# Optimization experiments

Hardware: AMD Instinct MI355X
Metric: run time of the kernel (lower is better)

Reference implementation:

```python
import jax, jax.numpy as jnp
import numpy as np

B, T, I, H = 256, 1024, 128, 256


def setup_inputs() -> dict:
    key = jax.random.key(0)
    ks = jax.random.split(key, 10)
    p = lambda k, shape: jax.random.normal(k, shape, dtype=jnp.float32) * 0.1
    return {
        "x": jax.random.normal(ks[0], (B, T, I), dtype=jnp.float32),
        # forget gate
        "f_wh": p(ks[1], (H, H)), "f_wx": p(ks[2], (I, H)), "f_b": p(ks[3], (H,)),
        # input (create) gate: potential (tanh) and percent (sigmoid) branches
        "i_wh_pot": p(ks[4], (H, H)), "i_wx_pot": p(ks[5], (I, H)), "i_b_pot": p(ks[6], (H,)),
        "i_wh_perc": p(ks[7], (H, H)), "i_wx_perc": p(ks[8], (I, H)), "i_b_perc": p(ks[9], (H,)),
        # output gate
        "o_wh": p(jax.random.fold_in(key, 10), (H, H)),
        "o_wx": p(jax.random.fold_in(key, 11), (I, H)),
        "o_b": p(jax.random.fold_in(key, 12), (H,)),
    }


def reference(x, f_wh, f_wx, f_b, i_wh_pot, i_wx_pot, i_b_pot,
              i_wh_perc, i_wx_perc, i_b_perc, o_wh, o_wx, o_b):
    # x: [B, T, I]
    sigmoid, tanh = jax.nn.sigmoid, jnp.tanh

    def step(carry, xt):  # xt: [B, I]
        s, l = carry  # short_term [B,H], long_term [B,H]
        forget = sigmoid(s @ f_wh + xt @ f_wx + f_b)
        create = sigmoid(s @ i_wh_perc + xt @ i_wx_perc + i_b_perc) * \
                 tanh(s @ i_wh_pot + xt @ i_wx_pot + i_b_pot)
        l_new = forget * l + create
        s_new = tanh(l_new) * sigmoid(s @ o_wh + xt @ o_wx + o_b)
        return (s_new, l_new), None

    init = (jnp.zeros((x.shape[0], f_b.shape[0]), x.dtype),
            jnp.zeros((x.shape[0], f_b.shape[0]), x.dtype))
    (short_term, long_term), _ = jax.lax.scan(step, init, jnp.swapaxes(x, 0, 1))
    return short_term, long_term
```

## Files before the change

kernel.cpp:

```cpp
#include <hip/hip_runtime.h>
#include <cstdint>

#define T_STEPS 1024
#define I_DIM 128
#define H_DIM 256

typedef __attribute__((ext_vector_type(8))) short bf16x8;
typedef __attribute__((ext_vector_type(4))) float f32x4;
typedef __attribute__((ext_vector_type(2))) unsigned int u32x2;

__device__ __forceinline__ uint32_t f2bf(float f) {
    uint32_t u = __builtin_bit_cast(uint32_t, f);
    return (u + 0x7FFFu + ((u >> 16) & 1u)) >> 16;
}
__device__ __forceinline__ uint32_t pk2bf(float lo, float hi) {
    return (f2bf(lo) & 0xFFFFu) | (f2bf(hi) << 16);
}
__device__ __forceinline__ float sigmoid_(float v) { return 1.f / (1.f + __expf(-v)); }
__device__ __forceinline__ float tanh_(float v) { float e = __expf(2.f * v); return 1.f - 2.f / (e + 1.f); }

__global__ void __launch_bounds__(256, 1)
lstm_kernel(const float* __restrict__ x,
            const float* __restrict__ f_wh, const float* __restrict__ f_wx, const float* __restrict__ f_b,
            const float* __restrict__ p_wh, const float* __restrict__ p_wx, const float* __restrict__ p_b,
            const float* __restrict__ c_wh, const float* __restrict__ c_wx, const float* __restrict__ c_b,
            const float* __restrict__ o_wh, const float* __restrict__ o_wx, const float* __restrict__ o_b,
            float* __restrict__ out, uint8_t* __restrict__ ws)
{
    __shared__ __align__(16) uint8_t lds[65792];
    uint8_t* WH = lds;
    uint8_t* WX = lds + 32768;
    uint8_t* SL = lds + 49152;
    uint8_t* XT = lds + 57344;
    float*   GB = (float*)(lds + 61440);

    const int tid  = (int)threadIdx.x;
    const int lane = tid & 63;
    const int wv   = tid >> 6;
    const int blk  = (int)blockIdx.x;
    const int grp  = blk & 15;
    const int cwg  = blk >> 4;
    const int grow0 = grp << 4;
    const int hc0   = cwg << 4;

    uint8_t* sbase = ws + 4096;

    const float* wh = (wv == 0) ? f_wh : (wv == 1) ? p_wh : (wv == 2) ? c_wh : o_wh;
    const float* wx = (wv == 0) ? f_wx : (wv == 1) ? p_wx : (wv == 2) ? c_wx : o_wx;
    const float* bp = (wv == 0) ? f_b  : (wv == 1) ? p_b  : (wv == 2) ? c_b  : o_b;

    {
        const int col = lane & 15, kc = lane >> 4;
        const uint32_t csw = (uint32_t)((col & 7) << 4);
        uint8_t* whb = WH + (size_t)(wv * 16 + col) * 512;
        #pragma unroll
        for (int it = 0; it < 8; ++it) {
            const int k0 = it * 32 + kc * 8;
            float v0 = wh[(size_t)(k0 + 0) * H_DIM + hc0 + col];
            float v1 = wh[(size_t)(k0 + 1) * H_DIM + hc0 + col];
            float v2 = wh[(size_t)(k0 + 2) * H_DIM + hc0 + col];
            float v3 = wh[(size_t)(k0 + 3) * H_DIM + hc0 + col];
            float v4 = wh[(size_t)(k0 + 4) * H_DIM + hc0 + col];
            float v5 = wh[(size_t)(k0 + 5) * H_DIM + hc0 + col];
            float v6 = wh[(size_t)(k0 + 6) * H_DIM + hc0 + col];
            float v7 = wh[(size_t)(k0 + 7) * H_DIM + hc0 + col];
            uint4 pk;
            pk.x = pk2bf(v0, v1); pk.y = pk2bf(v2, v3);
            pk.z = pk2bf(v4, v5); pk.w = pk2bf(v6, v7);
            *(uint4*)(whb + (((uint32_t)(it * 64 + kc * 16)) ^ csw)) = pk;
        }
        uint8_t* wxb = WX + (size_t)(wv * 16 + col) * 256;
        #pragma unroll
        for (int it = 0; it < 4; ++it) {
            const int k0 = it * 32 + kc * 8;
            float v0 = wx[(size_t)(k0 + 0) * H_DIM + hc0 + col];
            float v1 = wx[(size_t)(k0 + 1) * H_DIM + hc0 + col];
            float v2 = wx[(size_t)(k0 + 2) * H_DIM + hc0 + col];
            float v3 = wx[(size_t)(k0 + 3) * H_DIM + hc0 + col];
            float v4 = wx[(size_t)(k0 + 4) * H_DIM + hc0 + col];
            float v5 = wx[(size_t)(k0 + 5) * H_DIM + hc0 + col];
            float v6 = wx[(size_t)(k0 + 6) * H_DIM + hc0 + col];
            float v7 = wx[(size_t)(k0 + 7) * H_DIM + hc0 + col];
            uint4 pk;
            pk.x = pk2bf(v0, v1); pk.y = pk2bf(v2, v3);
            pk.z = pk2bf(v4, v5); pk.w = pk2bf(v6, v7);
            *(uint4*)(wxb + (((uint32_t)(it * 64 + kc * 16)) ^ csw)) = pk;
        }
    }
    const float bias = bp[hc0 + (lane & 15)];
    __syncthreads();

    const int fr = lane & 15, fkc = lane >> 4;
    const uint32_t fsw = (uint32_t)((fr & 7) << 4);
    uint8_t* slA = SL + (size_t)fr * 512;
    uint8_t* xtA = XT + (size_t)fr * 256;
    const uint8_t* whB = WH + (size_t)(wv * 16 + fr) * 512;
    const uint8_t* wxB = WX + (size_t)(wv * 16 + fr) * 256;

    uint4 bwh[8], bwx[4];
    #pragma unroll
    for (int q = 0; q < 8; ++q)
        bwh[q] = *(const uint4*)(whB + (((uint32_t)(q * 64 + fkc * 16)) ^ fsw));
    #pragma unroll
    for (int q = 0; q < 4; ++q)
        bwx[q] = *(const uint4*)(wxB + (((uint32_t)(q * 64 + fkc * 16)) ^ fsw));

    const int crow = tid >> 4, ccol = tid & 15;

    if ((tid & 1) == 0) {
        uint8_t* pdst = sbase + (size_t)(grow0 + crow) * 1024 + (size_t)(cwg * 8 + (ccol >> 1)) * 8;
        u32x2 pd; pd.x = 0u; pd.y = 1u;
        asm volatile("global_store_dwordx2 %0, %1, off sc0 sc1" :: "v"(pdst), "v"(pd) : "memory");
    }

    const int xrow = tid >> 4, xseg = tid & 15;
    const uint32_t xsw = (uint32_t)((xrow & 7) << 4);
    const float* xptr = x + (size_t)(grow0 + xrow) * (T_STEPS * I_DIM) + xseg * 8;
    float4 xr0 = *(const float4*)(xptr);
    float4 xr1 = *(const float4*)(xptr + 4);

    float l_reg = 0.f, s_fin = 0.f, l_fin = 0.f;

    for (int t = 0; t < T_STEPS; ++t) {
        {
            uint4 pk;
            pk.x = pk2bf(xr0.x, xr0.y); pk.y = pk2bf(xr0.z, xr0.w);
            pk.z = pk2bf(xr1.x, xr1.y); pk.w = pk2bf(xr1.z, xr1.w);
            *(uint4*)(XT + (size_t)xrow * 256 + (((uint32_t)(xseg * 16)) ^ xsw)) = pk;
        }
        {
            const int tn = (t + 1 < T_STEPS) ? (t + 1) : (T_STEPS - 1);
            const float* p = xptr + (size_t)tn * I_DIM;
            xr0 = *(const float4*)(p);
            xr1 = *(const float4*)(p + 4);
        }
        __syncthreads();

        f32x4 accA = {0.f, 0.f, 0.f, 0.f};
        #pragma unroll
        for (int q = 0; q < 4; ++q) {
            uint4 av = *(const uint4*)(xtA + (((uint32_t)(q * 64 + fkc * 16)) ^ fsw));
            accA = __builtin_amdgcn_mfma_f32_16x16x32_bf16(
                __builtin_bit_cast(bf16x8, av), __builtin_bit_cast(bf16x8, bwx[q]), accA, 0, 0, 0);
        }

        uint4 g0, g1, g2, g3;
        uint32_t m;
        const uint32_t e = (uint32_t)t + 1u;
        const uint8_t* src = sbase + (size_t)((t & 1) ? 262144 : 0)
                           + (size_t)(grow0 + xrow) * 1024 + (size_t)xseg * 64;
        do {
            asm volatile("global_load_dwordx4 %0, %1, off sc0 sc1"
                         : "=v"(g0) : "v"(src) : "memory");
            asm volatile("global_load_dwordx4 %0, %1, off offset:16 sc0 sc1"
                         : "=v"(g1) : "v"(src) : "memory");
            asm volatile("global_load_dwordx4 %0, %1, off offset:32 sc0 sc1"
                         : "=v"(g2) : "v"(src) : "memory");
            asm volatile("global_load_dwordx4 %0, %1, off offset:48 sc0 sc1"
                         : "=v"(g3) : "v"(src) : "memory");
            asm volatile("s_waitcnt vmcnt(0)" ::: "memory");
            __builtin_amdgcn_sched_barrier(0);
            m = (g0.y ^ e) | (g0.w ^ e) | (g1.y ^ e) | (g1.w ^ e)
              | (g2.y ^ e) | (g2.w ^ e) | (g3.y ^ e) | (g3.w ^ e);
        } while (m != 0);

        {
            uint4 d0; d0.x = g0.x; d0.y = g0.z; d0.z = g1.x; d0.w = g1.z;
            uint4 d1; d1.x = g2.x; d1.y = g2.z; d1.z = g3.x; d1.w = g3.z;
            uint8_t* dst = SL + (size_t)xrow * 512;
            const uint32_t o = (uint32_t)(xseg * 32);
            *(uint4*)(dst + (o ^ xsw)) = d0;
            *(uint4*)(dst + ((o + 16) ^ xsw)) = d1;
        }
        __syncthreads();

        f32x4 accB = {0.f, 0.f, 0.f, 0.f};
        #pragma unroll
        for (int q = 0; q < 4; ++q) {
            uint4 a0 = *(const uint4*)(slA + (((uint32_t)(q * 64 + fkc * 16)) ^ fsw));
            uint4 a1 = *(const uint4*)(slA + (((uint32_t)((q + 4) * 64 + fkc * 16)) ^ fsw));
            accA = __builtin_amdgcn_mfma_f32_16x16x32_bf16(
                __builtin_bit_cast(bf16x8, a0), __builtin_bit_cast(bf16x8, bwh[q]), accA, 0, 0, 0);
            accB = __builtin_amdgcn_mfma_f32_16x16x32_bf16(
                __builtin_bit_cast(bf16x8, a1), __builtin_bit_cast(bf16x8, bwh[q + 4]), accB, 0, 0, 0);
        }

        #pragma unroll
        for (int j = 0; j < 4; ++j) {
            const float pre = accA[j] + accB[j] + bias;
            const float a = (wv == 1) ? tanh_(pre) : sigmoid_(pre);
            GB[wv * 272 + (fkc * 4 + j) * 17 + fr] = a;
        }
        __syncthreads();

        {
            const float fg  = GB[0 * 272 + crow * 17 + ccol];
            const float pot = GB[1 * 272 + crow * 17 + ccol];
            const float prc = GB[2 * 272 + crow * 17 + ccol];
            const float og  = GB[3 * 272 + crow * 17 + ccol];
            const float lnew = fg * l_reg + prc * pot;
            const float snew = tanh_(lnew) * og;
            l_reg = lnew;
            if (t == T_STEPS - 1) { s_fin = snew; l_fin = lnew; }
            const uint32_t sb = f2bf(snew);
            const uint32_t ob = (uint32_t)__shfl_xor((int)sb, 1, 64);
            if (((tid & 1) == 0) && (t != T_STEPS - 1)) {
                uint8_t* pdst = sbase + (size_t)(((t + 1) & 1) ? 262144 : 0)
                              + (size_t)(grow0 + crow) * 1024 + (size_t)(cwg * 8 + (ccol >> 1)) * 8;
                u32x2 pd; pd.x = (sb & 0xFFFFu) | (ob << 16); pd.y = (uint32_t)t + 2u;
                asm volatile("global_store_dwordx2 %0, %1, off sc0 sc1" :: "v"(pdst), "v"(pd) : "memory");
            }
        }
    }

    out[(size_t)(grow0 + crow) * H_DIM + hc0 + ccol] = s_fin;
    out[(size_t)H_DIM * H_DIM + (size_t)(grow0 + crow) * H_DIM + hc0 + ccol] = l_fin;
}

extern "C" void kernel_launch(void* const* d_in, const int* in_sizes, int n_in,
                              void* d_out, int out_size, void* d_ws, size_t ws_size,
                              hipStream_t stream) {
    const float* x    = (const float*)d_in[0];
    const float* f_wh = (const float*)d_in[1];
    const float* f_wx = (const float*)d_in[2];
    const float* f_b  = (const float*)d_in[3];
    const float* p_wh = (const float*)d_in[4];
    const float* p_wx = (const float*)d_in[5];
    const float* p_b  = (const float*)d_in[6];
    const float* c_wh = (const float*)d_in[7];
    const float* c_wx = (const float*)d_in[8];
    const float* c_b  = (const float*)d_in[9];
    const float* o_wh = (const float*)d_in[10];
    const float* o_wx = (const float*)d_in[11];
    const float* o_b  = (const float*)d_in[12];
    float* outp = (float*)d_out;
    uint8_t* wsp = (uint8_t*)d_ws;

    hipMemsetAsync(d_ws, 0, 4096 + 2 * 262144, stream);

    void* args[] = { (void*)&x,
                     (void*)&f_wh, (void*)&f_wx, (void*)&f_b,
                     (void*)&p_wh, (void*)&p_wx, (void*)&p_b,
                     (void*)&c_wh, (void*)&c_wx, (void*)&c_b,
                     (void*)&o_wh, (void*)&o_wx, (void*)&o_b,
                     (void*)&outp, (void*)&wsp };
    hipLaunchCooperativeKernel((const void*)lstm_kernel, dim3(256), dim3(256), args, 0, stream);
}
```

Baseline: 1.947 ms.

## Collapse each block to one wavefront holding all four gate weights in registers

Each block now runs a single 64-lane wavefront that keeps bf16 weights for all four gates in VGPRs and computes every gate with MFMA directly. This removes the LDS staging, the gate exchange buffer and the three __syncthreads per timestep. The hidden state is loaded straight from the global tagged buffer into MFMA A-fragments, with x prefetch issued in the same batch and a wave-wide poll. It also switches from cooperative launch to a plain launch, which assumes all 256 single-wave blocks are co-resident. Register pressure rises sharply, and each step now serialises the x load latency with the state poll.

Result: slower. 4.297 ms (+120.7%).

```diff
diff --git a/kernel.cpp b/kernel.cpp
--- a/kernel.cpp
+++ b/kernel.cpp
@@ -16,10 +16,40 @@
 __device__ __forceinline__ uint32_t pk2bf(float lo, float hi) {
     return (f2bf(lo) & 0xFFFFu) | (f2bf(hi) << 16);
 }
+__device__ __forceinline__ float bcf(uint32_t u) { return __builtin_bit_cast(float, u); }
 __device__ __forceinline__ float sigmoid_(float v) { return 1.f / (1.f + __expf(-v)); }
 __device__ __forceinline__ float tanh_(float v) { float e = __expf(2.f * v); return 1.f - 2.f / (e + 1.f); }
 
-__global__ void __launch_bounds__(256, 1)
+#define TAGOR(e) ( (sg0.y^(e))|(sg0.w^(e))|(sg1.y^(e))|(sg1.w^(e)) \
+                 | (sg2.y^(e))|(sg2.w^(e))|(sg3.y^(e))|(sg3.w^(e)) \
+                 | (sg4.y^(e))|(sg4.w^(e))|(sg5.y^(e))|(sg5.w^(e)) \
+                 | (sg6.y^(e))|(sg6.w^(e))|(sg7.y^(e))|(sg7.w^(e)) \
+                 | (sg8.y^(e))|(sg8.w^(e))|(sg9.y^(e))|(sg9.w^(e)) \
+                 | (sg10.y^(e))|(sg10.w^(e))|(sg11.y^(e))|(sg11.w^(e)) \
+                 | (sg12.y^(e))|(sg12.w^(e))|(sg13.y^(e))|(sg13.w^(e)) \
+                 | (sg14.y^(e))|(sg14.w^(e))|(sg15.y^(e))|(sg15.w^(e)) )
+
+#define SMFMA(Q, A0, A1) do {                                                  \
+    uint4 af_; af_.x = (A0).x; af_.y = (A0).z; af_.z = (A1).x; af_.w = (A1).z; \
+    _Pragma("unroll")                                                          \
+    for (int g_ = 0; g_ < 4; ++g_)                                             \
+        acc[g_] = __builtin_amdgcn_mfma_f32_16x16x32_bf16(                     \
+            __builtin_bit_cast(bf16x8, af_), __builtin_bit_cast(bf16x8, bwh[g_][Q]), \
+            acc[g_], 0, 0, 0);                                                 \
+} while (0)
+
+#define XMFMA(Q, X0, X1) do {                                                  \
+    uint4 xf_;                                                                 \
+    xf_.x = pk2bf(bcf((X0).x), bcf((X0).y)); xf_.y = pk2bf(bcf((X0).z), bcf((X0).w)); \
+    xf_.z = pk2bf(bcf((X1).x), bcf((X1).y)); xf_.w = pk2bf(bcf((X1).z), bcf((X1).w)); \
+    _Pragma("unroll")                                                          \
+    for (int g_ = 0; g_ < 4; ++g_)                                             \
+        acc[g_] = __builtin_amdgcn_mfma_f32_16x16x32_bf16(                     \
+            __builtin_bit_cast(bf16x8, xf_), __builtin_bit_cast(bf16x8, bwx[g_][Q]), \
+            acc[g_], 0, 0, 0);                                                 \
+} while (0)
+
+__global__ void __launch_bounds__(64, 1)
 lstm_kernel(const float* __restrict__ x,
             const float* __restrict__ f_wh, const float* __restrict__ f_wx, const float* __restrict__ f_b,
             const float* __restrict__ p_wh, const float* __restrict__ p_wx, const float* __restrict__ p_b,
@@ -27,16 +57,9 @@
             const float* __restrict__ o_wh, const float* __restrict__ o_wx, const float* __restrict__ o_b,
             float* __restrict__ out, uint8_t* __restrict__ ws)
 {
-    __shared__ __align__(16) uint8_t lds[65792];
-    uint8_t* WH = lds;
-    uint8_t* WX = lds + 32768;
-    uint8_t* SL = lds + 49152;
-    uint8_t* XT = lds + 57344;
-    float*   GB = (float*)(lds + 61440);
-
-    const int tid  = (int)threadIdx.x;
-    const int lane = tid & 63;
-    const int wv   = tid >> 6;
+    const int lane = (int)threadIdx.x;
+    const int fr   = lane & 15;
+    const int fkc  = lane >> 4;
     const int blk  = (int)blockIdx.x;
     const int grp  = blk & 15;
     const int cwg  = blk >> 4;
@@ -45,176 +68,185 @@
 
     uint8_t* sbase = ws + 4096;
 
-    const float* wh = (wv == 0) ? f_wh : (wv == 1) ? p_wh : (wv == 2) ? c_wh : o_wh;
-    const float* wx = (wv == 0) ? f_wx : (wv == 1) ? p_wx : (wv == 2) ? c_wx : o_wx;
-    const float* bp = (wv == 0) ? f_b  : (wv == 1) ? p_b  : (wv == 2) ? c_b  : o_b;
-
-    {
-        const int col = lane & 15, kc = lane >> 4;
-        const uint32_t csw = (uint32_t)((col & 7) << 4);
-        uint8_t* whb = WH + (size_t)(wv * 16 + col) * 512;
-        #pragma unroll
-        for (int it = 0; it < 8; ++it) {
-            const int k0 = it * 32 + kc * 8;
-            float v0 = wh[(size_t)(k0 + 0) * H_DIM + hc0 + col];
-            float v1 = wh[(size_t)(k0 + 1) * H_DIM + hc0 + col];
-            float v2 = wh[(size_t)(k0 + 2) * H_DIM + hc0 + col];
-            float v3 = wh[(size_t)(k0 + 3) * H_DIM + hc0 + col];
-            float v4 = wh[(size_t)(k0 + 4) * H_DIM + hc0 + col];
-            float v5 = wh[(size_t)(k0 + 5) * H_DIM + hc0 + col];
-            float v6 = wh[(size_t)(k0 + 6) * H_DIM + hc0 + col];
-            float v7 = wh[(size_t)(k0 + 7) * H_DIM + hc0 + col];
-            uint4 pk;
-            pk.x = pk2bf(v0, v1); pk.y = pk2bf(v2, v3);
-            pk.z = pk2bf(v4, v5); pk.w = pk2bf(v6, v7);
-            *(uint4*)(whb + (((uint32_t)(it * 64 + kc * 16)) ^ csw)) = pk;
-        }
-        uint8_t* wxb = WX + (size_t)(wv * 16 + col) * 256;
-        #pragma unroll
-        for (int it = 0; it < 4; ++it) {
-            const int k0 = it * 32 + kc * 8;
-            float v0 = wx[(size_t)(k0 + 0) * H_DIM + hc0 + col];
-            float v1 = wx[(size_t)(k0 + 1) * H_DIM + hc0 + col];
-            float v2 = wx[(size_t)(k0 + 2) * H_DIM + hc0 + col];
-            float v3 = wx[(size_t)(k0 + 3) * H_DIM + hc0 + col];
-            float v4 = wx[(size_t)(k0 + 4) * H_DIM + hc0 + col];
-            float v5 = wx[(size_t)(k0 + 5) * H_DIM + hc0 + col];
-            float v6 = wx[(size_t)(k0 + 6) * H_DIM + hc0 + col];
-            float v7 = wx[(size_t)(k0 + 7) * H_DIM + hc0 + col];
-            uint4 pk;
-            pk.x = pk2bf(v0, v1); pk.y = pk2bf(v2, v3);
-            pk.z = pk2bf(v4, v5); pk.w = pk2bf(v6, v7);
-            *(uint4*)(wxb + (((uint32_t)(it * 64 + kc * 16)) ^ csw)) = pk;
-        }
-    }
-    const float bias = bp[hc0 + (lane & 15)];
-    __syncthreads();
-
-    const int fr = lane & 15, fkc = lane >> 4;
-    const uint32_t fsw = (uint32_t)((fr & 7) << 4);
-    uint8_t* slA = SL + (size_t)fr * 512;
-    uint8_t* xtA = XT + (size_t)fr * 256;
-    const uint8_t* whB = WH + (size_t)(wv * 16 + fr) * 512;
-    const uint8_t* wxB = WX + (size_t)(wv * 16 + fr) * 256;
-
-    uint4 bwh[8], bwx[4];
+    const float* whp[4] = { f_wh, p_wh, c_wh, o_wh };
+    const float* wxp[4] = { f_wx, p_wx, c_wx, o_wx };
+    const float* bpp[4] = { f_b,  p_b,  c_b,  o_b  };
+    uint4 bwh[4][8], bwx[4][4];
+    float bias4[4];
     #pragma unroll
-    for (int q = 0; q < 8; ++q)
-        bwh[q] = *(const uint4*)(whB + (((uint32_t)(q * 64 + fkc * 16)) ^ fsw));
+    for (int g = 0; g < 4; ++g) {
+        const float* W = whp[g];
+        #pragma unroll
+        for (int q = 0; q < 8; ++q) {
+            const int k0 = q * 32 + fkc * 8;
+            float v[8];
+            #pragma unroll
+            for (int i = 0; i < 8; ++i) v[i] = W[(size_t)(k0 + i) * H_DIM + hc0 + fr];
+            bwh[g][q].x = pk2bf(v[0], v[1]); bwh[g][q].y = pk2bf(v[2], v[3]);
+            bwh[g][q].z = pk2bf(v[4], v[5]); bwh[g][q].w = pk2bf(v[6], v[7]);
+        }
+        const float* Wx = wxp[g];
+        #pragma unroll
+        for (int q = 0; q < 4; ++q) {
+            const int k0 = q * 32 + fkc * 8;
+            float v[8];
+            #pragma unroll
+            for (int i = 0; i < 8; ++i) v[i] = Wx[(size_t)(k0 + i) * H_DIM + hc0 + fr];
+            bwx[g][q].x = pk2bf(v[0], v[1]); bwx[g][q].y = pk2bf(v[2], v[3]);
+            bwx[g][q].z = pk2bf(v[4], v[5]); bwx[g][q].w = pk2bf(v[6], v[7]);
+        }
+        bias4[g] = bpp[g][hc0 + fr];
+    }
+
+    const uint8_t* spA = sbase +          (size_t)(grow0 + fr) * 1024 + (size_t)fkc * 32;
+    const uint8_t* spB = sbase + 262144 + (size_t)(grow0 + fr) * 1024 + (size_t)fkc * 32;
+    uint8_t* pbA = sbase +          (size_t)(grow0 + fkc * 4) * 1024 + (size_t)(cwg * 8 + (fr >> 1)) * 8;
+    uint8_t* pbB = sbase + 262144 + (size_t)(grow0 + fkc * 4) * 1024 + (size_t)(cwg * 8 + (fr >> 1)) * 8;
+    const uint8_t* xcur = (const uint8_t*)(x + (size_t)(grow0 + fr) * (T_STEPS * I_DIM) + fkc * 8);
+
+    if ((lane & 1) == 0) {
+        u32x2 pd; pd.x = 0u; pd.y = 1u;
+        asm volatile(
+            "global_store_dwordx2 %[pb], %[pd], off sc0 sc1\n\t"
+            "global_store_dwordx2 %[pb], %[pd], off offset:1024 sc0 sc1\n\t"
+            "global_store_dwordx2 %[pb], %[pd], off offset:2048 sc0 sc1\n\t"
+            "global_store_dwordx2 %[pb], %[pd], off offset:3072 sc0 sc1"
+            :: [pb]"v"(pbA), [pd]"v"(pd) : "memory");
+    }
+
+    uint4 sg0, sg1, sg2, sg3, sg4, sg5, sg6, sg7;
+    uint4 sg8, sg9, sg10, sg11, sg12, sg13, sg14, sg15;
+    uint4 xr0, xr1, xr2, xr3, xr4, xr5, xr6, xr7;
+
+    float l_reg[4] = {0.f, 0.f, 0.f, 0.f};
+    float s_fin[4] = {0.f, 0.f, 0.f, 0.f};
+    float l_fin[4] = {0.f, 0.f, 0.f, 0.f};
+
+    for (int t = 0; t < T_STEPS; ++t) {
+        const uint32_t e = (uint32_t)t + 1u;
+        const uint8_t* sp = (t & 1) ? spB : spA;
+
+        asm volatile(
+            "global_load_dwordx4 %[g0], %[sp], off sc0 sc1\n\t"
+            "global_load_dwordx4 %[g1], %[sp], off offset:16 sc0 sc1\n\t"
+            "global_load_dwordx4 %[g2], %[sp], off offset:128 sc0 sc1\n\t"
+            "global_load_dwordx4 %[g3], %[sp], off offset:144 sc0 sc1\n\t"
+            "global_load_dwordx4 %[g4], %[sp], off offset:256 sc0 sc1\n\t"
+            "global_load_dwordx4 %[g5], %[sp], off offset:272 sc0 sc1\n\t"
+            "global_load_dwordx4 %[g6], %[sp], off offset:384 sc0 sc1\n\t"
+            "global_load_dwordx4 %[g7], %[sp], off offset:400 sc0 sc1\n\t"
+            "global_load_dwordx4 %[g8], %[sp], off offset:512 sc0 sc1\n\t"
+            "global_load_dwordx4 %[g9], %[sp], off offset:528 sc0 sc1\n\t"
+            "global_load_dwordx4 %[g10], %[sp], off offset:640 sc0 sc1\n\t"
+            "global_load_dwordx4 %[g11], %[sp], off offset:656 sc0 sc1\n\t"
+            "global_load_dwordx4 %[g12], %[sp], off offset:768 sc0 sc1\n\t"
+            "global_load_dwordx4 %[g13], %[sp], off offset:784 sc0 sc1\n\t"
+            "global_load_dwordx4 %[g14], %[sp], off offset:896 sc0 sc1\n\t"
+            "global_load_dwordx4 %[g15], %[sp], off offset:912 sc0 sc1\n\t"
+            "global_load_dwordx4 %[x0], %[xp], off\n\t"
+            "global_load_dwordx4 %[x1], %[xp], off offset:16\n\t"
+            "global_load_dwordx4 %[x2], %[xp], off offset:128\n\t"
+            "global_load_dwordx4 %[x3], %[xp], off offset:144\n\t"
+            "global_load_dwordx4 %[x4], %[xp], off offset:256\n\t"
+            "global_load_dwordx4 %[x5], %[xp], off offset:272\n\t"
+            "global_load_dwordx4 %[x6], %[xp], off offset:384\n\t"
+            "global_load_dwordx4 %[x7], %[xp], off offset:400\n\t"
+            "s_waitcnt vmcnt(0)"
+            : [g0]"=&v"(sg0), [g1]"=&v"(sg1), [g2]"=&v"(sg2), [g3]"=&v"(sg3),
+              [g4]"=&v"(sg4), [g5]"=&v"(sg5), [g6]"=&v"(sg6), [g7]"=&v"(sg7),
+              [g8]"=&v"(sg8), [g9]"=&v"(sg9), [g10]"=&v"(sg10), [g11]"=&v"(sg11),
+              [g12]"=&v"(sg12), [g13]"=&v"(sg13), [g14]"=&v"(sg14), [g15]"=&v"(sg15),
+              [x0]"=&v"(xr0), [x1]"=&v"(xr1), [x2]"=&v"(xr2), [x3]"=&v"(xr3),
+              [x4]"=&v"(xr4), [x5]"=&v"(xr5), [x6]"=&v"(xr6), [x7]"=&v"(xr7)
+            : [sp]"v"(sp), [xp]"v"(xcur)
+            : "memory");
+
+        uint32_t m = TAGOR(e);
+        while (__any(m != 0)) {
+            asm volatile(
+                "global_load_dwordx4 %[g0], %[sp], off sc0 sc1\n\t"
+                "global_load_dwordx4 %[g1], %[sp], off offset:16 sc0 sc1\n\t"
+                "global_load_dwordx4 %[g2], %[sp], off offset:128 sc0 sc1\n\t"
+                "global_load_dwordx4 %[g3], %[sp], off offset:144 sc0 sc1\n\t"
+                "global_load_dwordx4 %[g4], %[sp], off offset:256 sc0 sc1\n\t"
+                "global_load_dwordx4 %[g5], %[sp], off offset:272 sc0 sc1\n\t"
+                "global_load_dwordx4 %[g6], %[sp], off offset:384 sc0 sc1\n\t"
+                "global_load_dwordx4 %[g7], %[sp], off offset:400 sc0 sc1\n\t"
+                "global_load_dwordx4 %[g8], %[sp], off offset:512 sc0 sc1\n\t"
+                "global_load_dwordx4 %[g9], %[sp], off offset:528 sc0 sc1\n\t"
+                "global_load_dwordx4 %[g10], %[sp], off offset:640 sc0 sc1\n\t"
+                "global_load_dwordx4 %[g11], %[sp], off offset:656 sc0 sc1\n\t"
+                "global_load_dwordx4 %[g12], %[sp], off offset:768 sc0 sc1\n\t"
+                "global_load_dwordx4 %[g13], %[sp], off offset:784 sc0 sc1\n\t"
+                "global_load_dwordx4 %[g14], %[sp], off offset:896 sc0 sc1\n\t"
+                "global_load_dwordx4 %[g15], %[sp], off offset:912 sc0 sc1\n\t"
+                "s_waitcnt vmcnt(0)"
+                : [g0]"=&v"(sg0), [g1]"=&v"(sg1), [g2]"=&v"(sg2), [g3]"=&v"(sg3),
+                  [g4]"=&v"(sg4), [g5]"=&v"(sg5), [g6]"=&v"(sg6), [g7]"=&v"(sg7),
+                  [g8]"=&v"(sg8), [g9]"=&v"(sg9), [g10]"=&v"(sg10), [g11]"=&v"(sg11),
+                  [g12]"=&v"(sg12), [g13]"=&v"(sg13), [g14]"=&v"(sg14), [g15]"=&v"(sg15)
+                : [sp]"v"(sp)
+                : "memory");
+            m = TAGOR(e);
+        }
+
+        f32x4 acc[4];
+        #pragma unroll
+        for (int g = 0; g < 4; ++g) acc[g] = (f32x4){0.f, 0.f, 0.f, 0.f};
+        XMFMA(0, xr0, xr1); XMFMA(1, xr2, xr3); XMFMA(2, xr4, xr5); XMFMA(3, xr6, xr7);
+        SMFMA(0, sg0, sg1);  SMFMA(1, sg2, sg3);  SMFMA(2, sg4, sg5);  SMFMA(3, sg6, sg7);
+        SMFMA(4, sg8, sg9);  SMFMA(5, sg10, sg11); SMFMA(6, sg12, sg13); SMFMA(7, sg14, sg15);
+
+        float snew[4];
+        #pragma unroll
+        for (int j = 0; j < 4; ++j) {
+            const float fg  = sigmoid_(acc[0][j] + bias4[0]);
+            const float pot = tanh_   (acc[1][j] + bias4[1]);
+            const float prc = sigmoid_(acc[2][j] + bias4[2]);
+            const float og  = sigmoid_(acc[3][j] + bias4[3]);
+            const float lnew = fg * l_reg[j] + prc * pot;
+            snew[j] = tanh_(lnew) * og;
+            l_reg[j] = lnew;
+        }
+        if (t == T_STEPS - 1) {
+            #pragma unroll
+            for (int j = 0; j < 4; ++j) { s_fin[j] = snew[j]; l_fin[j] = l_reg[j]; }
+            break;
+        }
+
+        uint32_t sb0 = f2bf(snew[0]), sb1 = f2bf(snew[1]);
+        uint32_t sb2 = f2bf(snew[2]), sb3 = f2bf(snew[3]);
+        uint32_t ob0 = (uint32_t)__shfl_xor((int)sb0, 1, 64);
+        uint32_t ob1 = (uint32_t)__shfl_xor((int)sb1, 1, 64);
+        uint32_t ob2 = (uint32_t)__shfl_xor((int)sb2, 1, 64);
+        uint32_t ob3 = (uint32_t)__shfl_xor((int)sb3, 1, 64);
+
+        {
+            uint8_t* pb = ((t + 1) & 1) ? pbB : pbA;
+            const uint32_t tg = (uint32_t)t + 2u;
+            if ((lane & 1) == 0) {
+                u32x2 p0; p0.x = (sb0 & 0xFFFFu) | (ob0 << 16); p0.y = tg;
+                u32x2 p1; p1.x = (sb1 & 0xFFFFu) | (ob1 << 16); p1.y = tg;
+                u32x2 p2; p2.x = (sb2 & 0xFFFFu) | (ob2 << 16); p2.y = tg;
+                u32x2 p3; p3.x = (sb3 & 0xFFFFu) | (ob3 << 16); p3.y = tg;
+                asm volatile(
+                    "global_store_dwordx2 %[pb], %[p0], off sc0 sc1\n\t"
+                    "global_store_dwordx2 %[pb], %[p1], off offset:1024 sc0 sc1\n\t"
+                    "global_store_dwordx2 %[pb], %[p2], off offset:2048 sc0 sc1\n\t"
+                    "global_store_dwordx2 %[pb], %[p3], off offset:3072 sc0 sc1"
+                    :: [pb]"v"(pb), [p0]"v"(p0), [p1]"v"(p1), [p2]"v"(p2), [p3]"v"(p3)
+                    : "memory");
+            }
+        }
+        xcur += 512;
+    }
+
     #pragma unroll
-    for (int q = 0; q < 4; ++q)
-        bwx[q] = *(const uint4*)(wxB + (((uint32_t)(q * 64 + fkc * 16)) ^ fsw));
-
-    const int crow = tid >> 4, ccol = tid & 15;
-
-    if ((tid & 1) == 0) {
-        uint8_t* pdst = sbase + (size_t)(grow0 + crow) * 1024 + (size_t)(cwg * 8 + (ccol >> 1)) * 8;
-        u32x2 pd; pd.x = 0u; pd.y = 1u;
-        asm volatile("global_store_dwordx2 %0, %1, off sc0 sc1" :: "v"(pdst), "v"(pd) : "memory");
-    }
-
-    const int xrow = tid >> 4, xseg = tid & 15;
-    const uint32_t xsw = (uint32_t)((xrow & 7) << 4);
-    const float* xptr = x + (size_t)(grow0 + xrow) * (T_STEPS * I_DIM) + xseg * 8;
-    float4 xr0 = *(const float4*)(xptr);
-    float4 xr1 = *(const float4*)(xptr + 4);
-
-    float l_reg = 0.f, s_fin = 0.f, l_fin = 0.f;
-
-    for (int t = 0; t < T_STEPS; ++t) {
-        {
-            uint4 pk;
-            pk.x = pk2bf(xr0.x, xr0.y); pk.y = pk2bf(xr0.z, xr0.w);
-            pk.z = pk2bf(xr1.x, xr1.y); pk.w = pk2bf(xr1.z, xr1.w);
-            *(uint4*)(XT + (size_t)xrow * 256 + (((uint32_t)(xseg * 16)) ^ xsw)) = pk;
-        }
-        {
-            const int tn = (t + 1 < T_STEPS) ? (t + 1) : (T_STEPS - 1);
-            const float* p = xptr + (size_t)tn * I_DIM;
-            xr0 = *(const float4*)(p);
-            xr1 = *(const float4*)(p + 4);
-        }
-        __syncthreads();
-
-        f32x4 accA = {0.f, 0.f, 0.f, 0.f};
-        #pragma unroll
-        for (int q = 0; q < 4; ++q) {
-            uint4 av = *(const uint4*)(xtA + (((uint32_t)(q * 64 + fkc * 16)) ^ fsw));
-            accA = __builtin_amdgcn_mfma_f32_16x16x32_bf16(
-                __builtin_bit_cast(bf16x8, av), __builtin_bit_cast(bf16x8, bwx[q]), accA, 0, 0, 0);
-        }
-
-        uint4 g0, g1, g2, g3;
-        uint32_t m;
-        const uint32_t e = (uint32_t)t + 1u;
-        const uint8_t* src = sbase + (size_t)((t & 1) ? 262144 : 0)
-                           + (size_t)(grow0 + xrow) * 1024 + (size_t)xseg * 64;
-        do {
-            asm volatile("global_load_dwordx4 %0, %1, off sc0 sc1"
-                         : "=v"(g0) : "v"(src) : "memory");
-            asm volatile("global_load_dwordx4 %0, %1, off offset:16 sc0 sc1"
-                         : "=v"(g1) : "v"(src) : "memory");
-            asm volatile("global_load_dwordx4 %0, %1, off offset:32 sc0 sc1"
-                         : "=v"(g2) : "v"(src) : "memory");
-            asm volatile("global_load_dwordx4 %0, %1, off offset:48 sc0 sc1"
-                         : "=v"(g3) : "v"(src) : "memory");
-            asm volatile("s_waitcnt vmcnt(0)" ::: "memory");
-            __builtin_amdgcn_sched_barrier(0);
-            m = (g0.y ^ e) | (g0.w ^ e) | (g1.y ^ e) | (g1.w ^ e)
-              | (g2.y ^ e) | (g2.w ^ e) | (g3.y ^ e) | (g3.w ^ e);
-        } while (m != 0);
-
-        {
-            uint4 d0; d0.x = g0.x; d0.y = g0.z; d0.z = g1.x; d0.w = g1.z;
-            uint4 d1; d1.x = g2.x; d1.y = g2.z; d1.z = g3.x; d1.w = g3.z;
-            uint8_t* dst = SL + (size_t)xrow * 512;
-            const uint32_t o = (uint32_t)(xseg * 32);
-            *(uint4*)(dst + (o ^ xsw)) = d0;
-            *(uint4*)(dst + ((o + 16) ^ xsw)) = d1;
-        }
-        __syncthreads();
-
-        f32x4 accB = {0.f, 0.f, 0.f, 0.f};
-        #pragma unroll
-        for (int q = 0; q < 4; ++q) {
-            uint4 a0 = *(const uint4*)(slA + (((uint32_t)(q * 64 + fkc * 16)) ^ fsw));
-            uint4 a1 = *(const uint4*)(slA + (((uint32_t)((q + 4) * 64 + fkc * 16)) ^ fsw));
-            accA = __builtin_amdgcn_mfma_f32_16x16x32_bf16(
-                __builtin_bit_cast(bf16x8, a0), __builtin_bit_cast(bf16x8, bwh[q]), accA, 0, 0, 0);
-            accB = __builtin_amdgcn_mfma_f32_16x16x32_bf16(
-                __builtin_bit_cast(bf16x8, a1), __builtin_bit_cast(bf16x8, bwh[q + 4]), accB, 0, 0, 0);
-        }
-
-        #pragma unroll
-        for (int j = 0; j < 4; ++j) {
-            const float pre = accA[j] + accB[j] + bias;
-            const float a = (wv == 1) ? tanh_(pre) : sigmoid_(pre);
-            GB[wv * 272 + (fkc * 4 + j) * 17 + fr] = a;
-        }
-        __syncthreads();
-
-        {
-            const float fg  = GB[0 * 272 + crow * 17 + ccol];
-            const float pot = GB[1 * 272 + crow * 17 + ccol];
-            const float prc = GB[2 * 272 + crow * 17 + ccol];
-            const float og  = GB[3 * 272 + crow * 17 + ccol];
-            const float lnew = fg * l_reg + prc * pot;
-            const float snew = tanh_(lnew) * og;
-            l_reg = lnew;
-            if (t == T_STEPS - 1) { s_fin = snew; l_fin = lnew; }
-            const uint32_t sb = f2bf(snew);
-            const uint32_t ob = (uint32_t)__shfl_xor((int)sb, 1, 64);
-            if (((tid & 1) == 0) && (t != T_STEPS - 1)) {
-                uint8_t* pdst = sbase + (size_t)(((t + 1) & 1) ? 262144 : 0)
-                              + (size_t)(grow0 + crow) * 1024 + (size_t)(cwg * 8 + (ccol >> 1)) * 8;
-                u32x2 pd; pd.x = (sb & 0xFFFFu) | (ob << 16); pd.y = (uint32_t)t + 2u;
-                asm volatile("global_store_dwordx2 %0, %1, off sc0 sc1" :: "v"(pdst), "v"(pd) : "memory");
-            }
-        }
-    }
-
-    out[(size_t)(grow0 + crow) * H_DIM + hc0 + ccol] = s_fin;
-    out[(size_t)H_DIM * H_DIM + (size_t)(grow0 + crow) * H_DIM + hc0 + ccol] = l_fin;
+    for (int j = 0; j < 4; ++j) {
+        const size_t row = (size_t)(grow0 + fkc * 4 + j);
+        out[row * H_DIM + hc0 + fr] = s_fin[j];
+        out[(size_t)H_DIM * H_DIM + row * H_DIM + hc0 + fr] = l_fin[j];
+    }
 }
 
 extern "C" void kernel_launch(void* const* d_in, const int* in_sizes, int n_in,
@@ -238,11 +270,6 @@
 
     hipMemsetAsync(d_ws, 0, 4096 + 2 * 262144, stream);
 
-    void* args[] = { (void*)&x,
-                     (void*)&f_wh, (void*)&f_wx, (void*)&f_b,
-                     (void*)&p_wh, (void*)&p_wx, (void*)&p_b,
-                     (void*)&c_wh, (void*)&c_wx, (void*)&c_b,
-                     (void*)&o_wh, (void*)&o_wx, (void*)&o_b,
-                     (void*)&outp, (void*)&wsp };
-    hipLaunchCooperativeKernel((const void*)lstm_kernel, dim3(256), dim3(256), args, 0, stream);
-}
+    lstm_kernel<<<dim3(256), dim3(64), 0, stream>>>(
+        x, f_wh, f_wx, f_b, p_wh, p_wx, p_b, c_wh, c_wx, c_b, o_wh, o_wx, o_b, outp, wsp);
+}
```
